# Kernel optimization log

Measured on AMD Instinct MI355X. Metric: run time of the kernel, lower is better.

The kernel has to match this reference:

```python
import jax, jax.numpy as jnp
import numpy as np

B, S, H = 16, 4096, 4096
NH, NKV, HD = 32, 8, 128
NREP = NH // NKV
EPS = 1e-5


def _rmsnorm(x, eps=EPS):
    xf = x.astype(jnp.float32)
    return (xf * jax.lax.rsqrt(jnp.mean(xf * xf, axis=-1, keepdims=True) + eps)).astype(x.dtype)


def setup_inputs() -> dict:
    key = jax.random.key(0)
    ks = jax.random.split(key, 8)
    x = jax.random.normal(ks[0], (B, 1, H), dtype=jnp.float32)
    last_pos = jax.random.randint(ks[1], (B,), 0, S)
    # rope cache: [max_seq, head_dim//2, 2] = stacked (cos, sin)
    inv_freq = 1.0 / (10000.0 ** (jnp.arange(0, HD, 2, dtype=jnp.float32) / HD))  # [HD//2]
    t = jnp.arange(S, dtype=jnp.float32)
    ang = t[:, None] * inv_freq[None, :]  # [S, HD//2]
    rope_cache = jnp.stack([jnp.cos(ang), jnp.sin(ang)], axis=-1)  # [S, HD//2, 2]
    mask = jnp.ones((B, 1, 1, S), dtype=bool)
    sc = 1.0 / np.sqrt(H)
    wqkv = jax.random.normal(ks[2], ((NH + 2 * NKV) * HD, H), dtype=jnp.float32) * sc
    o_proj_w = jax.random.normal(ks[3], (H, NH * HD), dtype=jnp.float32) * sc
    cache_k = jax.random.normal(ks[4], (B, S, NKV, HD), dtype=jnp.float32)
    cache_v = jax.random.normal(ks[5], (B, S, NKV, HD), dtype=jnp.float32)
    return {"x": x, "last_pos": last_pos, "rope_cache": rope_cache, "mask": mask,
            "wqkv": wqkv, "o_proj_w": o_proj_w, "cache_k": cache_k, "cache_v": cache_v}


def _rope_decode(x, last_pos, rope_cache):
    # x: [B, 1, nh, HD]; rope_cache: [S, HD//2, 2]; last_pos: [B]
    rc = rope_cache[last_pos]  # [B, HD//2, 2] gathered per position
    rc = rc[:, None, None, :, :]  # [B,1,1,HD//2,2]
    xs = x.astype(jnp.float32).reshape(*x.shape[:-1], HD // 2, 2)
    real = xs[..., 0] * rc[..., 0] - xs[..., 1] * rc[..., 1]
    imag = xs[..., 1] * rc[..., 0] + xs[..., 0] * rc[..., 1]
    return jnp.stack([real, imag], axis=-1).reshape(x.shape).astype(x.dtype)


def reference(x, last_pos, rope_cache, mask, wqkv, o_proj_w, cache_k, cache_v):
    bsz = x.shape[0]
    qkv = jnp.einsum('bsh,oh->bso', x, wqkv)  # [B,1,(NH+2*NKV)*HD]
    q_end = NH * HD
    k_end = q_end + NKV * HD
    q = qkv[..., :q_end].reshape(bsz, 1, NH, HD)
    k = qkv[..., q_end:k_end].reshape(bsz, 1, NKV, HD)
    v = qkv[..., k_end:].reshape(bsz, 1, NKV, HD)
    # RoPE at position last_pos (decode path: start_pos = last_pos)
    q = _rope_decode(q, last_pos, rope_cache)
    k = _rope_decode(k, last_pos, rope_cache)
    # QK RMSNorm over head_dim
    q = _rmsnorm(q)
    k = _rmsnorm(k)
    # scatter new K/V into cache at last_pos
    b_idx = jnp.arange(bsz)
    keys = cache_k.at[b_idx, last_pos].set(k[:, 0])    # [B,S,NKV,HD]
    values = cache_v.at[b_idx, last_pos].set(v[:, 0])  # [B,S,NKV,HD]
    # GQA attention without materializing repeat_interleave:
    # head h uses kv group h // NREP, so reshape heads -> [NKV, NREP]
    qg = q[:, 0].reshape(bsz, NKV, NREP, HD)
    scores = jnp.einsum('bgrd,bsgd->bgrs', qg, keys) / np.sqrt(HD)  # [B,NKV,NREP,S]
    neg = jnp.finfo(scores.dtype).min
    scores = jnp.where(mask, scores, neg)  # mask [B,1,1,S] broadcasts
    probs = jax.nn.softmax(scores.astype(jnp.float32), axis=-1).astype(q.dtype)
    out = jnp.einsum('bgrs,bsgd->bgrd', probs, values)  # [B,NKV,NREP,HD]
    out = out.reshape(bsz, 1, NH * HD)
    return jnp.einsum('bso,ho->bsh', out, o_proj_w)  # [B,1,H]
```

## Files before the change

kernel.cpp:

```cpp
#include <hip/hip_runtime.h>
#include <hip/hip_bf16.h>

#define BATCH   16
#define SEQ     4096
#define HID     4096
#define NHEADS  32
#define NKVH    8
#define HDIM    128
#define NREPS   4
#define QKV_DIM 6144
#define NSCH    16
#define SCH     256

__device__ __forceinline__ void gload16(float* lds, const float* g) {
  __builtin_amdgcn_global_load_lds(
      (const __attribute__((address_space(1))) unsigned int*)g,
      (__attribute__((address_space(3))) unsigned int*)lds,
      16, 0, 0);
}
#define WAITV(N) asm volatile("s_waitcnt vmcnt(" #N ")" ::: "memory")

__global__ __launch_bounds__(256) void gemv16(
    const float4* __restrict__ x4,
    const float4* __restrict__ w4,
    float* __restrict__ ypart,
    int M)
{
  const int wid  = threadIdx.x >> 6;
  const int lane = threadIdx.x & 63;
  const int mb   = M / 16;
  const int ks   = blockIdx.x / mb;
  const int rb   = blockIdx.x % mb;
  const int row0 = rb * 16 + wid * 4;
  const int k0   = ks * 512;

  float acc[16][4];
#pragma unroll
  for (int b = 0; b < 16; ++b) { acc[b][0]=0.f; acc[b][1]=0.f; acc[b][2]=0.f; acc[b][3]=0.f; }

  for (int c = 0; c < 512; c += 64) {
    const int kk = k0 + c + lane;
    const long wb = (long)row0 * 1024 + kk;
    float4 w0 = w4[wb];
    float4 w1 = w4[wb + 1024];
    float4 w2 = w4[wb + 2048];
    float4 w3 = w4[wb + 3072];
    float4 xv[16];
#pragma unroll
    for (int b = 0; b < 16; ++b) xv[b] = x4[(b << 10) + kk];
#pragma unroll
    for (int b = 0; b < 16; ++b) {
      acc[b][0] = fmaf(w0.x,xv[b].x,fmaf(w0.y,xv[b].y,fmaf(w0.z,xv[b].z,fmaf(w0.w,xv[b].w,acc[b][0]))));
      acc[b][1] = fmaf(w1.x,xv[b].x,fmaf(w1.y,xv[b].y,fmaf(w1.z,xv[b].z,fmaf(w1.w,xv[b].w,acc[b][1]))));
      acc[b][2] = fmaf(w2.x,xv[b].x,fmaf(w2.y,xv[b].y,fmaf(w2.z,xv[b].z,fmaf(w2.w,xv[b].w,acc[b][2]))));
      acc[b][3] = fmaf(w3.x,xv[b].x,fmaf(w3.y,xv[b].y,fmaf(w3.z,xv[b].z,fmaf(w3.w,xv[b].w,acc[b][3]))));
    }
  }
#pragma unroll
  for (int b = 0; b < 16; ++b) {
#pragma unroll
    for (int r = 0; r < 4; ++r) {
      float v = acc[b][r];
#pragma unroll
      for (int o = 32; o; o >>= 1) v += __shfl_xor(v, o, 64);
      if (lane == 0) ypart[((long)(ks * 16 + b)) * M + row0 + r] = v;
    }
  }
}

__global__ __launch_bounds__(64) void rope_rms(
    const float*  __restrict__ qp0,
    const float*  __restrict__ qp1,
    const int*    __restrict__ last_pos,
    const float2* __restrict__ rope2,
    float* __restrict__ proc)
{
  const int b    = blockIdx.x / 48;
  const int hh   = blockIdx.x % 48;
  const int lane = threadIdx.x;
  const int off  = b * QKV_DIM + hh * HDIM;

  float2 e0 = ((const float2*)(qp0 + off))[lane];
  float2 e1 = ((const float2*)(qp1 + off))[lane];
  float ex = e0.x + e1.x, ey = e0.y + e1.y;
  float r0 = ex, r1 = ey;
  if (hh < 40) {
    const int pos = last_pos[b];
    float2 cs = rope2[pos * 64 + lane];
    r0 = ex * cs.x - ey * cs.y;
    r1 = ey * cs.x + ex * cs.y;
    float ss = r0 * r0 + r1 * r1;
#pragma unroll
    for (int o = 32; o; o >>= 1) ss += __shfl_xor(ss, o, 64);
    float scl = rsqrtf(ss * (1.0f / 128.0f) + 1e-5f);
    r0 *= scl; r1 *= scl;
  }
  ((float2*)(proc + off))[lane] = make_float2(r0, r1);
}

__global__ __launch_bounds__(256, 4) void attn_partial(
    const float* __restrict__ proc,
    const float* __restrict__ cache_k,
    const float* __restrict__ cache_v,
    const int*   __restrict__ last_pos,
    float* __restrict__ part_out,
    float* __restrict__ part_ml)
{
  __shared__ float smem[8192];
  __shared__ float sc[NREPS][SCH];
  __shared__ float red[NREPS][8];

  const int ch  = blockIdx.x & (NSCH - 1);
  const int g   = (blockIdx.x >> 4) & 7;
  const int b   = blockIdx.x >> 7;
  const int tid = threadIdx.x;
  const int w   = tid >> 6;
  const int hw  = tid >> 5;
  const int h   = hw & 1;
  const int sub = tid & 31;
  const int r   = sub >> 3;
  const int sl  = sub & 7;
  const int pos = last_pos[b];
  const int s0  = ch * SCH;

  const float* kbase = cache_k + ((long)(b * SEQ) * NKVH + g) * HDIM;
  const float* vbase = cache_v + ((long)(b * SEQ) * NKVH + g) * HDIM;
  const float* knew  = proc + b * QKV_DIM + (NHEADS + g) * HDIM;
  const float* vnew  = proc + b * QKV_DIM + (NHEADS + NKVH + g) * HDIM;

  const float isq = 0.08838834764831845f;
  float4 ql[4];
#pragma unroll
  for (int t = 0; t < 4; ++t) {
    float4 q = *(const float4*)(proc + b * QKV_DIM + (g * NREPS + r) * HDIM + sl * 16 + t * 4);
    ql[t] = make_float4(q.x * isq, q.y * isq, q.z * isq, q.w * isq);
  }
  WAITV(0);

#define STAGE_K(tt, bf) do {                                                 \
    float* dst_ = &smem[((w * 2 + (bf)) * 8) * 128];                         \
    _Pragma("unroll")                                                        \
    for (int c_ = 0; c_ < 4; ++c_) {                                         \
      const int s_ = s0 + (w << 6) + ((tt) << 3) + (c_ << 1) + h;            \
      const float* src_ = (s_ == pos) ? (knew + (sub << 2))                  \
                                      : (kbase + (long)s_ * 1024 + (sub << 2)); \
      gload16(dst_ + (c_ << 8), src_);                                       \
    }                                                                        \
  } while (0)

#define STAGE_V(tt, bf) do {                                                 \
    float* dst_ = &smem[((w * 2 + (bf)) * 4) * 128];                         \
    { const int s_ = s0 + (w << 6) + ((tt) << 1) + h;                        \
      const float* src_ = (s_ == pos) ? (vnew + (sub << 2))                  \
                                      : (vbase + (long)s_ * 1024 + (sub << 2)); \
      gload16(dst_, src_); }                                                 \
    { const int s_ = s0 + (w << 6) + 32 + ((tt) << 1) + h;                   \
      const float* src_ = (s_ == pos) ? (vnew + (sub << 2))                  \
                                      : (vbase + (long)s_ * 1024 + (sub << 2)); \
      gload16(dst_ + 256, src_); }                                           \
  } while (0)

  STAGE_K(0, 0);
  STAGE_K(1, 1);
  float m = -3e38f;
  for (int tt = 0; tt < 8; ++tt) {
    if (tt < 7) WAITV(4); else WAITV(0);
    const float* kb = &smem[((w * 2 + (tt & 1)) * 8) * 128];
#pragma unroll
    for (int pp = 0; pp < 4; ++pp) {
      const int p = (pp << 1) + h;
      const float4 k0 = *(const float4*)&kb[p * 128 + sl * 16];
      const float4 k1 = *(const float4*)&kb[p * 128 + sl * 16 + 4];
      const float4 k2 = *(const float4*)&kb[p * 128 + sl * 16 + 8];
      const float4 k3 = *(const float4*)&kb[p * 128 + sl * 16 + 12];
      float d = k0.x*ql[0].x + k0.y*ql[0].y + k0.z*ql[0].z + k0.w*ql[0].w
              + k1.x*ql[1].x + k1.y*ql[1].y + k1.z*ql[1].z + k1.w*ql[1].w
              + k2.x*ql[2].x + k2.y*ql[2].y + k2.z*ql[2].z + k2.w*ql[2].w
              + k3.x*ql[3].x + k3.y*ql[3].y + k3.z*ql[3].z + k3.w*ql[3].w;
      d += __shfl_xor(d, 1); d += __shfl_xor(d, 2); d += __shfl_xor(d, 4);
      const int i = (w << 6) + (tt << 3) + p;
      if (sl == 0) sc[r][i] = d;
      m = fmaxf(m, d);
    }
    if (tt < 6) STAGE_K(tt + 2, tt & 1);
  }
  if (sl == 0) red[r][hw] = m;
  __syncthreads();

  STAGE_V(0, 0);
  STAGE_V(1, 1);

  float m_r[4];
#pragma unroll
  for (int r2 = 0; r2 < 4; ++r2) {
    float mm = red[r2][0];
#pragma unroll
    for (int h2 = 1; h2 < 8; ++h2) mm = fmaxf(mm, red[r2][h2]);
    m_r[r2] = mm;
  }

  float lsum[4];
  {
    const int i = tid;
#pragma unroll
    for (int r2 = 0; r2 < 4; ++r2) {
      float e = __expf(sc[r2][i] - m_r[r2]);
      sc[r2][i] = e;
      lsum[r2] = e;
    }
  }
  __syncthreads();
  const int wid  = tid >> 6;
  const int lane = tid & 63;
#pragma unroll
  for (int r2 = 0; r2 < 4; ++r2) {
    float v = lsum[r2];
#pragma unroll
    for (int o = 32; o; o >>= 1) v += __shfl_xor(v, o, 64);
    if (lane == 0) red[r2][wid] = v;
  }
  __syncthreads();
  float l_r[4];
#pragma unroll
  for (int r2 = 0; r2 < 4; ++r2)
    l_r[r2] = (red[r2][0] + red[r2][1]) + (red[r2][2] + red[r2][3]);

  float* ps = &smem[4096];
  const int dq = sub;
  float4 a0 = {0,0,0,0}, a1 = {0,0,0,0}, a2 = {0,0,0,0}, a3 = {0,0,0,0};
  for (int tt = 0; tt < 16; ++tt) {
    if (tt < 15) WAITV(2); else WAITV(0);
    const float* vb = &smem[((w * 2 + (tt & 1)) * 4) * 128];
#pragma unroll
    for (int j = 0; j < 2; ++j) {
      const int i = (w << 6) + (h << 5) + (tt << 1) + j;
      const float4 vv = *(const float4*)&vb[(h * 2 + j) * 128 + (dq << 2)];
      const float p0 = sc[0][i], p1 = sc[1][i], p2 = sc[2][i], p3 = sc[3][i];
      a0.x += p0*vv.x; a0.y += p0*vv.y; a0.z += p0*vv.z; a0.w += p0*vv.w;
      a1.x += p1*vv.x; a1.y += p1*vv.y; a1.z += p1*vv.z; a1.w += p1*vv.w;
      a2.x += p2*vv.x; a2.y += p2*vv.y; a2.z += p2*vv.z; a2.w += p2*vv.w;
      a3.x += p3*vv.x; a3.y += p3*vv.y; a3.z += p3*vv.z; a3.w += p3*vv.w;
    }
    if (tt < 14) STAGE_V(tt + 2, tt & 1);
  }
  *(float4*)&ps[(long)hw * 512 + 0 * 128 + (dq << 2)] = a0;
  *(float4*)&ps[(long)hw * 512 + 1 * 128 + (dq << 2)] = a1;
  *(float4*)&ps[(long)hw * 512 + 2 * 128 + (dq << 2)] = a2;
  *(float4*)&ps[(long)hw * 512 + 3 * 128 + (dq << 2)] = a3;
  __syncthreads();

  const long base = ((((long)b * NKVH + g) * NSCH + ch) * NREPS) * HDIM;
  for (int idx = tid; idx < 512; idx += 256) {
    float v = 0.f;
#pragma unroll
    for (int s2 = 0; s2 < 8; ++s2) v += ps[(long)s2 * 512 + idx];
    part_out[base + idx] = v;
  }
  if (tid < 4) {
    float mm = tid==0 ? m_r[0] : tid==1 ? m_r[1] : tid==2 ? m_r[2] : m_r[3];
    float ll = tid==0 ? l_r[0] : tid==1 ? l_r[1] : tid==2 ? l_r[2] : l_r[3];
    const long mlb = (((((long)b * NKVH + g) * NSCH + ch) * NREPS) + tid) * 2;
    part_ml[mlb]     = mm;
    part_ml[mlb + 1] = ll;
  }
#undef STAGE_K
#undef STAGE_V
}

__global__ __launch_bounds__(128) void attn_combine(
    const float* __restrict__ part_out,
    const float* __restrict__ part_ml,
    float* __restrict__ attn_out)
{
  const int r = blockIdx.x & 3;
  const int g = (blockIdx.x >> 2) & 7;
  const int b = blockIdx.x >> 5;
  const int d = threadIdx.x;

  float M = -3e38f;
#pragma unroll
  for (int c = 0; c < NSCH; ++c) {
    const long idx = ((((long)b * NKVH + g) * NSCH + c) * NREPS + r) * 2;
    M = fmaxf(M, part_ml[idx]);
  }
  float L = 0.f, o = 0.f;
#pragma unroll
  for (int c = 0; c < NSCH; ++c) {
    const long idx = ((((long)b * NKVH + g) * NSCH + c) * NREPS + r) * 2;
    const float w = __expf(part_ml[idx] - M);
    L += part_ml[idx + 1] * w;
    o += w * part_out[((((long)b * NKVH + g) * NSCH + c) * NREPS + r) * HDIM + d];
  }
  attn_out[((long)b * NHEADS + g * NREPS + r) * HDIM + d] = o / L;
}

__global__ __launch_bounds__(256) void gemv_oproj(
    const float4* __restrict__ x4,
    const float4* __restrict__ w4,
    float* __restrict__ out)
{
  const int wid  = threadIdx.x >> 6;
  const int lane = threadIdx.x & 63;
  const int row0 = blockIdx.x * 8 + wid * 2;

  float acc[16][2];
#pragma unroll
  for (int b = 0; b < 16; ++b) { acc[b][0] = 0.f; acc[b][1] = 0.f; }

  for (int c = 0; c < 1024; c += 64) {
    const int kk = c + lane;
    const long wb = (long)row0 * 1024 + kk;
    float4 w0 = w4[wb];
    float4 w1 = w4[wb + 1024];
    float4 xv[16];
#pragma unroll
    for (int b = 0; b < 16; ++b) xv[b] = x4[(b << 10) + kk];
#pragma unroll
    for (int b = 0; b < 16; ++b) {
      acc[b][0] = fmaf(w0.x,xv[b].x,fmaf(w0.y,xv[b].y,fmaf(w0.z,xv[b].z,fmaf(w0.w,xv[b].w,acc[b][0]))));
      acc[b][1] = fmaf(w1.x,xv[b].x,fmaf(w1.y,xv[b].y,fmaf(w1.z,xv[b].z,fmaf(w1.w,xv[b].w,acc[b][1]))));
    }
  }
#pragma unroll
  for (int b = 0; b < 16; ++b) {
#pragma unroll
    for (int r = 0; r < 2; ++r) {
      float v = acc[b][r];
#pragma unroll
      for (int o = 32; o; o >>= 1) v += __shfl_xor(v, o, 64);
      if (lane == 0) out[((long)b << 12) + row0 + r] = v;
    }
  }
}

extern "C" void kernel_launch(void* const* d_in, const int* in_sizes, int n_in,
                              void* d_out, int out_size, void* d_ws, size_t ws_size,
                              hipStream_t stream) {
  const float* x          = (const float*)d_in[0];
  const int*   last_pos   = (const int*)  d_in[1];
  const float* rope_cache = (const float*)d_in[2];
  const float* wqkv       = (const float*)d_in[4];
  const float* o_proj_w   = (const float*)d_in[5];
  const float* cache_k    = (const float*)d_in[6];
  const float* cache_v    = (const float*)d_in[7];
  float* out = (float*)d_out;
  float* ws  = (float*)d_ws;

  float* qkv_part = ws;
  float* proc     = ws + 196608;
  float* part_out = ws + 294912;
  float* part_ml  = ws + 1343488;
  float* attn_out = ws + 1359872;

  gemv16<<<(QKV_DIM / 16) * 2, 256, 0, stream>>>(
      (const float4*)x, (const float4*)wqkv, qkv_part, QKV_DIM);
  rope_rms<<<BATCH * 48, 64, 0, stream>>>(
      qkv_part, qkv_part + BATCH * QKV_DIM, last_pos,
      (const float2*)rope_cache, proc);
  attn_partial<<<BATCH * NKVH * NSCH, 256, 0, stream>>>(
      proc, cache_k, cache_v, last_pos, part_out, part_ml);
  attn_combine<<<BATCH * NKVH * NREPS, 128, 0, stream>>>(
      part_out, part_ml, attn_out);
  gemv_oproj<<<HID / 8, 256, 0, stream>>>(
      (const float4*)attn_out, (const float4*)o_proj_w, out);
}
```

Measured before the change: 208.6 us.

## Make each wave an independent attention split to remove block-level syncs

Each wave in the attention partial kernel now processes its own 64-position chunk with private staging buffers and score storage. Max and sum reductions use wave shuffles instead of shared-memory barriers, and V prefetch starts during the last K iterations. Partial results per wave are written out, so the combine kernel merges 64 chunks instead of 16. This removes __syncthreads and the cross-wave LDS reduction, at the cost of four times more partial output traffic and more combine work.

```diff
diff --git a/kernel.cpp b/kernel.cpp
--- a/kernel.cpp
+++ b/kernel.cpp
@@ -10,7 +10,7 @@
 #define NREPS   4
 #define QKV_DIM 6144
 #define NSCH    16
-#define SCH     256
+#define NCHW    64
 
 __device__ __forceinline__ void gload16(float* lds, const float* g) {
   __builtin_amdgcn_global_load_lds(
@@ -106,22 +106,24 @@
     float* __restrict__ part_out,
     float* __restrict__ part_ml)
 {
-  __shared__ float smem[8192];
-  __shared__ float sc[NREPS][SCH];
-  __shared__ float red[NREPS][8];
+  __shared__ float stage[4][2][1024];
+  __shared__ float scb[4][NREPS][64];
 
   const int ch  = blockIdx.x & (NSCH - 1);
   const int g   = (blockIdx.x >> 4) & 7;
   const int b   = blockIdx.x >> 7;
   const int tid = threadIdx.x;
   const int w   = tid >> 6;
-  const int hw  = tid >> 5;
-  const int h   = hw & 1;
+  const int h   = (tid >> 5) & 1;
   const int sub = tid & 31;
   const int r   = sub >> 3;
   const int sl  = sub & 7;
   const int pos = last_pos[b];
-  const int s0  = ch * SCH;
+  const int s0  = (ch << 8) + (w << 6);
+  const int chw = (ch << 2) + w;
+
+  float* kv = &stage[w][0][0];
+  float (*sc)[64] = scb[w];
 
   const float* kbase = cache_k + ((long)(b * SEQ) * NKVH + g) * HDIM;
   const float* vbase = cache_v + ((long)(b * SEQ) * NKVH + g) * HDIM;
@@ -132,139 +134,111 @@
   float4 ql[4];
 #pragma unroll
   for (int t = 0; t < 4; ++t) {
-    float4 q = *(const float4*)(proc + b * QKV_DIM + (g * NREPS + r) * HDIM + sl * 16 + t * 4);
+    float4 q = *(const float4*)(proc + b * QKV_DIM + (g * NREPS + r) * HDIM + t * 32 + sl * 4);
     ql[t] = make_float4(q.x * isq, q.y * isq, q.z * isq, q.w * isq);
   }
   WAITV(0);
 
-#define STAGE_K(tt, bf) do {                                                 \
-    float* dst_ = &smem[((w * 2 + (bf)) * 8) * 128];                         \
+#define STAGE(base_, new_, tt, bf) do {                                      \
+    float* dst_ = kv + (bf) * 1024;                                          \
     _Pragma("unroll")                                                        \
     for (int c_ = 0; c_ < 4; ++c_) {                                         \
-      const int s_ = s0 + (w << 6) + ((tt) << 3) + (c_ << 1) + h;            \
-      const float* src_ = (s_ == pos) ? (knew + (sub << 2))                  \
-                                      : (kbase + (long)s_ * 1024 + (sub << 2)); \
+      const int s_ = s0 + ((tt) << 3) + (h << 2) + c_;                       \
+      const float* src_ = (s_ == pos) ? ((new_) + (sub << 2))                \
+                                      : ((base_) + (long)s_ * 1024 + (sub << 2)); \
       gload16(dst_ + (c_ << 8), src_);                                       \
     }                                                                        \
   } while (0)
 
-#define STAGE_V(tt, bf) do {                                                 \
-    float* dst_ = &smem[((w * 2 + (bf)) * 4) * 128];                         \
-    { const int s_ = s0 + (w << 6) + ((tt) << 1) + h;                        \
-      const float* src_ = (s_ == pos) ? (vnew + (sub << 2))                  \
-                                      : (vbase + (long)s_ * 1024 + (sub << 2)); \
-      gload16(dst_, src_); }                                                 \
-    { const int s_ = s0 + (w << 6) + 32 + ((tt) << 1) + h;                   \
-      const float* src_ = (s_ == pos) ? (vnew + (sub << 2))                  \
-                                      : (vbase + (long)s_ * 1024 + (sub << 2)); \
-      gload16(dst_ + 256, src_); }                                           \
-  } while (0)
-
-  STAGE_K(0, 0);
-  STAGE_K(1, 1);
+  STAGE(kbase, knew, 0, 0);
+  STAGE(kbase, knew, 1, 1);
   float m = -3e38f;
+#pragma unroll
   for (int tt = 0; tt < 8; ++tt) {
-    if (tt < 7) WAITV(4); else WAITV(0);
-    const float* kb = &smem[((w * 2 + (tt & 1)) * 8) * 128];
+    WAITV(4);
+    const float* kb = kv + (tt & 1) * 1024;
 #pragma unroll
     for (int pp = 0; pp < 4; ++pp) {
-      const int p = (pp << 1) + h;
-      const float4 k0 = *(const float4*)&kb[p * 128 + sl * 16];
-      const float4 k1 = *(const float4*)&kb[p * 128 + sl * 16 + 4];
-      const float4 k2 = *(const float4*)&kb[p * 128 + sl * 16 + 8];
-      const float4 k3 = *(const float4*)&kb[p * 128 + sl * 16 + 12];
+      const float* row = kb + pp * 256 + h * 128 + sl * 4;
+      float4 k0 = *(const float4*)(row);
+      float4 k1 = *(const float4*)(row + 32);
+      float4 k2 = *(const float4*)(row + 64);
+      float4 k3 = *(const float4*)(row + 96);
       float d = k0.x*ql[0].x + k0.y*ql[0].y + k0.z*ql[0].z + k0.w*ql[0].w
               + k1.x*ql[1].x + k1.y*ql[1].y + k1.z*ql[1].z + k1.w*ql[1].w
               + k2.x*ql[2].x + k2.y*ql[2].y + k2.z*ql[2].z + k2.w*ql[2].w
               + k3.x*ql[3].x + k3.y*ql[3].y + k3.z*ql[3].z + k3.w*ql[3].w;
       d += __shfl_xor(d, 1); d += __shfl_xor(d, 2); d += __shfl_xor(d, 4);
-      const int i = (w << 6) + (tt << 3) + p;
-      if (sl == 0) sc[r][i] = d;
+      if (sl == 0) sc[r][(tt << 3) + (h << 2) + pp] = d;
       m = fmaxf(m, d);
     }
-    if (tt < 6) STAGE_K(tt + 2, tt & 1);
-  }
-  if (sl == 0) red[r][hw] = m;
-  __syncthreads();
-
-  STAGE_V(0, 0);
-  STAGE_V(1, 1);
-
-  float m_r[4];
-#pragma unroll
-  for (int r2 = 0; r2 < 4; ++r2) {
-    float mm = red[r2][0];
-#pragma unroll
-    for (int h2 = 1; h2 < 8; ++h2) mm = fmaxf(mm, red[r2][h2]);
-    m_r[r2] = mm;
-  }
-
-  float lsum[4];
+    if (tt < 6)      STAGE(kbase, knew, tt + 2, tt & 1);
+    else             STAGE(vbase, vnew, tt - 6, tt & 1);
+  }
+
+  m = fmaxf(m, __shfl_xor(m, 32));
+  m = fmaxf(m, __shfl_xor(m, 1));
+  m = fmaxf(m, __shfl_xor(m, 2));
+  m = fmaxf(m, __shfl_xor(m, 4));
+
+  float lsum;
   {
-    const int i = tid;
-#pragma unroll
-    for (int r2 = 0; r2 < 4; ++r2) {
-      float e = __expf(sc[r2][i] - m_r[r2]);
-      sc[r2][i] = e;
-      lsum[r2] = e;
-    }
-  }
-  __syncthreads();
-  const int wid  = tid >> 6;
-  const int lane = tid & 63;
-#pragma unroll
-  for (int r2 = 0; r2 < 4; ++r2) {
-    float v = lsum[r2];
-#pragma unroll
-    for (int o = 32; o; o >>= 1) v += __shfl_xor(v, o, 64);
-    if (lane == 0) red[r2][wid] = v;
-  }
-  __syncthreads();
-  float l_r[4];
-#pragma unroll
-  for (int r2 = 0; r2 < 4; ++r2)
-    l_r[r2] = (red[r2][0] + red[r2][1]) + (red[r2][2] + red[r2][3]);
-
-  float* ps = &smem[4096];
+    const int i0 = (sl << 3) + (h << 2);
+    float4 e4 = *(const float4*)&sc[r][i0];
+    e4.x = __expf(e4.x - m); e4.y = __expf(e4.y - m);
+    e4.z = __expf(e4.z - m); e4.w = __expf(e4.w - m);
+    *(float4*)&sc[r][i0] = e4;
+    lsum = (e4.x + e4.y) + (e4.z + e4.w);
+  }
+  lsum += __shfl_xor(lsum, 32);
+  lsum += __shfl_xor(lsum, 1);
+  lsum += __shfl_xor(lsum, 2);
+  lsum += __shfl_xor(lsum, 4);
+
+  if (h == 0 && sl == 0) {
+    const long mlb = ((((long)(b * NKVH + g)) * NCHW + chw) * NREPS + r) * 2;
+    part_ml[mlb]     = m;
+    part_ml[mlb + 1] = lsum;
+  }
+
   const int dq = sub;
   float4 a0 = {0,0,0,0}, a1 = {0,0,0,0}, a2 = {0,0,0,0}, a3 = {0,0,0,0};
-  for (int tt = 0; tt < 16; ++tt) {
-    if (tt < 15) WAITV(2); else WAITV(0);
-    const float* vb = &smem[((w * 2 + (tt & 1)) * 4) * 128];
-#pragma unroll
-    for (int j = 0; j < 2; ++j) {
-      const int i = (w << 6) + (h << 5) + (tt << 1) + j;
-      const float4 vv = *(const float4*)&vb[(h * 2 + j) * 128 + (dq << 2)];
-      const float p0 = sc[0][i], p1 = sc[1][i], p2 = sc[2][i], p3 = sc[3][i];
-      a0.x += p0*vv.x; a0.y += p0*vv.y; a0.z += p0*vv.z; a0.w += p0*vv.w;
-      a1.x += p1*vv.x; a1.y += p1*vv.y; a1.z += p1*vv.z; a1.w += p1*vv.w;
-      a2.x += p2*vv.x; a2.y += p2*vv.y; a2.z += p2*vv.z; a2.w += p2*vv.w;
-      a3.x += p3*vv.x; a3.y += p3*vv.y; a3.z += p3*vv.z; a3.w += p3*vv.w;
-    }
-    if (tt < 14) STAGE_V(tt + 2, tt & 1);
-  }
-  *(float4*)&ps[(long)hw * 512 + 0 * 128 + (dq << 2)] = a0;
-  *(float4*)&ps[(long)hw * 512 + 1 * 128 + (dq << 2)] = a1;
-  *(float4*)&ps[(long)hw * 512 + 2 * 128 + (dq << 2)] = a2;
-  *(float4*)&ps[(long)hw * 512 + 3 * 128 + (dq << 2)] = a3;
-  __syncthreads();
-
-  const long base = ((((long)b * NKVH + g) * NSCH + ch) * NREPS) * HDIM;
-  for (int idx = tid; idx < 512; idx += 256) {
-    float v = 0.f;
-#pragma unroll
-    for (int s2 = 0; s2 < 8; ++s2) v += ps[(long)s2 * 512 + idx];
-    part_out[base + idx] = v;
-  }
-  if (tid < 4) {
-    float mm = tid==0 ? m_r[0] : tid==1 ? m_r[1] : tid==2 ? m_r[2] : m_r[3];
-    float ll = tid==0 ? l_r[0] : tid==1 ? l_r[1] : tid==2 ? l_r[2] : l_r[3];
-    const long mlb = (((((long)b * NKVH + g) * NSCH + ch) * NREPS) + tid) * 2;
-    part_ml[mlb]     = mm;
-    part_ml[mlb + 1] = ll;
-  }
-#undef STAGE_K
-#undef STAGE_V
+#pragma unroll
+  for (int tt = 0; tt < 8; ++tt) {
+    if (tt < 7) WAITV(4); else WAITV(0);
+    const float* vb = kv + (tt & 1) * 1024;
+    const int i0 = (tt << 3) + (h << 2);
+    const float4 p0 = *(const float4*)&sc[0][i0];
+    const float4 p1 = *(const float4*)&sc[1][i0];
+    const float4 p2 = *(const float4*)&sc[2][i0];
+    const float4 p3 = *(const float4*)&sc[3][i0];
+#pragma unroll
+    for (int c = 0; c < 4; ++c) {
+      const float4 vv = *(const float4*)(vb + c * 256 + h * 128 + (dq << 2));
+      const float q0 = ((const float*)&p0)[c];
+      const float q1 = ((const float*)&p1)[c];
+      const float q2 = ((const float*)&p2)[c];
+      const float q3 = ((const float*)&p3)[c];
+      a0.x += q0*vv.x; a0.y += q0*vv.y; a0.z += q0*vv.z; a0.w += q0*vv.w;
+      a1.x += q1*vv.x; a1.y += q1*vv.y; a1.z += q1*vv.z; a1.w += q1*vv.w;
+      a2.x += q2*vv.x; a2.y += q2*vv.y; a2.z += q2*vv.z; a2.w += q2*vv.w;
+      a3.x += q3*vv.x; a3.y += q3*vv.y; a3.z += q3*vv.z; a3.w += q3*vv.w;
+    }
+    if (tt < 6) STAGE(vbase, vnew, tt + 2, tt & 1);
+  }
+
+#pragma unroll
+  for (int k = 0; k < 4; ++k) {
+    float4* ak = k==0 ? &a0 : k==1 ? &a1 : k==2 ? &a2 : &a3;
+    ak->x += __shfl_xor(ak->x, 32);
+    ak->y += __shfl_xor(ak->y, 32);
+    ak->z += __shfl_xor(ak->z, 32);
+    ak->w += __shfl_xor(ak->w, 32);
+  }
+  float* pb = part_out + ((((long)(b * NKVH + g)) * NCHW + chw) * NREPS) * HDIM + (dq << 2);
+  *(float4*)(pb + (h * 2 + 0) * HDIM) = h ? a2 : a0;
+  *(float4*)(pb + (h * 2 + 1) * HDIM) = h ? a3 : a1;
+#undef STAGE
 }
 
 __global__ __launch_bounds__(128) void attn_combine(
@@ -276,20 +250,20 @@
   const int g = (blockIdx.x >> 2) & 7;
   const int b = blockIdx.x >> 5;
   const int d = threadIdx.x;
+  const long gb = (long)(b * NKVH + g);
 
   float M = -3e38f;
-#pragma unroll
-  for (int c = 0; c < NSCH; ++c) {
-    const long idx = ((((long)b * NKVH + g) * NSCH + c) * NREPS + r) * 2;
-    M = fmaxf(M, part_ml[idx]);
-  }
+#pragma unroll 8
+  for (int c = 0; c < NCHW; ++c)
+    M = fmaxf(M, part_ml[((gb * NCHW + c) * NREPS + r) * 2]);
+
   float L = 0.f, o = 0.f;
-#pragma unroll
-  for (int c = 0; c < NSCH; ++c) {
-    const long idx = ((((long)b * NKVH + g) * NSCH + c) * NREPS + r) * 2;
-    const float w = __expf(part_ml[idx] - M);
-    L += part_ml[idx + 1] * w;
-    o += w * part_out[((((long)b * NKVH + g) * NSCH + c) * NREPS + r) * HDIM + d];
+#pragma unroll 8
+  for (int c = 0; c < NCHW; ++c) {
+    const long idx = ((gb * NCHW + c) * NREPS + r) * 2;
+    const float wgt = __expf(part_ml[idx] - M);
+    L += part_ml[idx + 1] * wgt;
+    o += wgt * part_out[((gb * NCHW + c) * NREPS + r) * HDIM + d];
   }
   attn_out[((long)b * NHEADS + g * NREPS + r) * HDIM + d] = o / L;
 }
@@ -349,8 +323,8 @@
   float* qkv_part = ws;
   float* proc     = ws + 196608;
   float* part_out = ws + 294912;
-  float* part_ml  = ws + 1343488;
-  float* attn_out = ws + 1359872;
+  float* part_ml  = ws + 4489216;
+  float* attn_out = ws + 4554752;
 
   gemv16<<<(QKV_DIM / 16) * 2, 256, 0, stream>>>(
       (const float4*)x, (const float4*)wqkv, qkv_part, QKV_DIM);
```

Measured after the change: 259.4 us. 1.24x slower.

## Stage GEMV activations in LDS and split K four ways for both projections

Applied to the files above, without the earlier changes.

The QKV GEMV now stages the 16-batch activation slice in shared memory, so each wave reads it from LDS instead of issuing 16 global float4 loads per step. K is split into four chunks of 1024 instead of two, which doubles the grid, and rope_rms sums four partials. The o_proj GEMV reuses the same split-K kernel, followed by a new add4 reduction kernel. This buys more parallelism and less redundant activation traffic, at the cost of an extra launch and extra partial-sum traffic.

```diff
diff --git a/kernel.cpp b/kernel.cpp
--- a/kernel.cpp
+++ b/kernel.cpp
@@ -20,40 +20,46 @@
 }
 #define WAITV(N) asm volatile("s_waitcnt vmcnt(" #N ")" ::: "memory")
 
-__global__ __launch_bounds__(256) void gemv16(
+__global__ __launch_bounds__(256) void gemv_ldsx(
     const float4* __restrict__ x4,
     const float4* __restrict__ w4,
     float* __restrict__ ypart,
     int M)
 {
+  constexpr int KC4 = 256;
+  __shared__ float4 xs[16][KC4];
   const int wid  = threadIdx.x >> 6;
   const int lane = threadIdx.x & 63;
   const int mb   = M / 16;
   const int ks   = blockIdx.x / mb;
   const int rb   = blockIdx.x % mb;
   const int row0 = rb * 16 + wid * 4;
-  const int k0   = ks * 512;
+  const int k0   = ks * KC4;
+
+#pragma unroll
+  for (int i = threadIdx.x; i < 16 * KC4; i += 256)
+    xs[i >> 8][i & 255] = x4[((i >> 8) << 10) + k0 + (i & 255)];
+  __syncthreads();
 
   float acc[16][4];
 #pragma unroll
   for (int b = 0; b < 16; ++b) { acc[b][0]=0.f; acc[b][1]=0.f; acc[b][2]=0.f; acc[b][3]=0.f; }
 
-  for (int c = 0; c < 512; c += 64) {
+#pragma unroll
+  for (int c = 0; c < KC4; c += 64) {
     const int kk = k0 + c + lane;
     const long wb = (long)row0 * 1024 + kk;
     float4 w0 = w4[wb];
     float4 w1 = w4[wb + 1024];
     float4 w2 = w4[wb + 2048];
     float4 w3 = w4[wb + 3072];
-    float4 xv[16];
-#pragma unroll
-    for (int b = 0; b < 16; ++b) xv[b] = x4[(b << 10) + kk];
 #pragma unroll
     for (int b = 0; b < 16; ++b) {
-      acc[b][0] = fmaf(w0.x,xv[b].x,fmaf(w0.y,xv[b].y,fmaf(w0.z,xv[b].z,fmaf(w0.w,xv[b].w,acc[b][0]))));
-      acc[b][1] = fmaf(w1.x,xv[b].x,fmaf(w1.y,xv[b].y,fmaf(w1.z,xv[b].z,fmaf(w1.w,xv[b].w,acc[b][1]))));
-      acc[b][2] = fmaf(w2.x,xv[b].x,fmaf(w2.y,xv[b].y,fmaf(w2.z,xv[b].z,fmaf(w2.w,xv[b].w,acc[b][2]))));
-      acc[b][3] = fmaf(w3.x,xv[b].x,fmaf(w3.y,xv[b].y,fmaf(w3.z,xv[b].z,fmaf(w3.w,xv[b].w,acc[b][3]))));
+      float4 xv = xs[b][c + lane];
+      acc[b][0] = fmaf(w0.x,xv.x,fmaf(w0.y,xv.y,fmaf(w0.z,xv.z,fmaf(w0.w,xv.w,acc[b][0]))));
+      acc[b][1] = fmaf(w1.x,xv.x,fmaf(w1.y,xv.y,fmaf(w1.z,xv.z,fmaf(w1.w,xv.w,acc[b][1]))));
+      acc[b][2] = fmaf(w2.x,xv.x,fmaf(w2.y,xv.y,fmaf(w2.z,xv.z,fmaf(w2.w,xv.w,acc[b][2]))));
+      acc[b][3] = fmaf(w3.x,xv.x,fmaf(w3.y,xv.y,fmaf(w3.z,xv.z,fmaf(w3.w,xv.w,acc[b][3]))));
     }
   }
 #pragma unroll
@@ -68,9 +74,8 @@
   }
 }
 
-__global__ __launch_bounds__(64) void rope_rms(
-    const float*  __restrict__ qp0,
-    const float*  __restrict__ qp1,
+__global__ __launch_bounds__(64) void rope_rms4(
+    const float*  __restrict__ qp,
     const int*    __restrict__ last_pos,
     const float2* __restrict__ rope2,
     float* __restrict__ proc)
@@ -80,9 +85,12 @@
   const int lane = threadIdx.x;
   const int off  = b * QKV_DIM + hh * HDIM;
 
-  float2 e0 = ((const float2*)(qp0 + off))[lane];
-  float2 e1 = ((const float2*)(qp1 + off))[lane];
-  float ex = e0.x + e1.x, ey = e0.y + e1.y;
+  float ex = 0.f, ey = 0.f;
+#pragma unroll
+  for (int s = 0; s < 4; ++s) {
+    float2 t = ((const float2*)(qp + (long)s * BATCH * QKV_DIM + off))[lane];
+    ex += t.x; ey += t.y;
+  }
   float r0 = ex, r1 = ey;
   if (hh < 40) {
     const int pos = last_pos[b];
@@ -294,42 +302,14 @@
   attn_out[((long)b * NHEADS + g * NREPS + r) * HDIM + d] = o / L;
 }
 
-__global__ __launch_bounds__(256) void gemv_oproj(
-    const float4* __restrict__ x4,
-    const float4* __restrict__ w4,
-    float* __restrict__ out)
-{
-  const int wid  = threadIdx.x >> 6;
-  const int lane = threadIdx.x & 63;
-  const int row0 = blockIdx.x * 8 + wid * 2;
-
-  float acc[16][2];
-#pragma unroll
-  for (int b = 0; b < 16; ++b) { acc[b][0] = 0.f; acc[b][1] = 0.f; }
-
-  for (int c = 0; c < 1024; c += 64) {
-    const int kk = c + lane;
-    const long wb = (long)row0 * 1024 + kk;
-    float4 w0 = w4[wb];
-    float4 w1 = w4[wb + 1024];
-    float4 xv[16];
-#pragma unroll
-    for (int b = 0; b < 16; ++b) xv[b] = x4[(b << 10) + kk];
-#pragma unroll
-    for (int b = 0; b < 16; ++b) {
-      acc[b][0] = fmaf(w0.x,xv[b].x,fmaf(w0.y,xv[b].y,fmaf(w0.z,xv[b].z,fmaf(w0.w,xv[b].w,acc[b][0]))));
-      acc[b][1] = fmaf(w1.x,xv[b].x,fmaf(w1.y,xv[b].y,fmaf(w1.z,xv[b].z,fmaf(w1.w,xv[b].w,acc[b][1]))));
-    }
-  }
-#pragma unroll
-  for (int b = 0; b < 16; ++b) {
-#pragma unroll
-    for (int r = 0; r < 2; ++r) {
-      float v = acc[b][r];
-#pragma unroll
-      for (int o = 32; o; o >>= 1) v += __shfl_xor(v, o, 64);
-      if (lane == 0) out[((long)b << 12) + row0 + r] = v;
-    }
+__global__ __launch_bounds__(256) void add4(
+    const float4* __restrict__ p, float4* __restrict__ o, int n4)
+{
+  int i = blockIdx.x * 256 + threadIdx.x;
+  if (i < n4) {
+    float4 a = p[i], b = p[i + n4], c = p[i + 2 * n4], d = p[i + 3 * n4];
+    o[i] = make_float4(a.x+b.x+c.x+d.x, a.y+b.y+c.y+d.y,
+                       a.z+b.z+c.z+d.z, a.w+b.w+c.w+d.w);
   }
 }
 
@@ -347,20 +327,22 @@
   float* ws  = (float*)d_ws;
 
   float* qkv_part = ws;
-  float* proc     = ws + 196608;
-  float* part_out = ws + 294912;
-  float* part_ml  = ws + 1343488;
-  float* attn_out = ws + 1359872;
-
-  gemv16<<<(QKV_DIM / 16) * 2, 256, 0, stream>>>(
+  float* proc     = ws + 393216;
+  float* part_out = ws + 491520;
+  float* part_ml  = ws + 1540096;
+  float* attn_out = ws + 1556480;
+  float* out_part = ws + 1622016;
+
+  gemv_ldsx<<<(QKV_DIM / 16) * 4, 256, 0, stream>>>(
       (const float4*)x, (const float4*)wqkv, qkv_part, QKV_DIM);
-  rope_rms<<<BATCH * 48, 64, 0, stream>>>(
-      qkv_part, qkv_part + BATCH * QKV_DIM, last_pos,
-      (const float2*)rope_cache, proc);
+  rope_rms4<<<BATCH * 48, 64, 0, stream>>>(
+      qkv_part, last_pos, (const float2*)rope_cache, proc);
   attn_partial<<<BATCH * NKVH * NSCH, 256, 0, stream>>>(
       proc, cache_k, cache_v, last_pos, part_out, part_ml);
   attn_combine<<<BATCH * NKVH * NREPS, 128, 0, stream>>>(
       part_out, part_ml, attn_out);
-  gemv_oproj<<<HID / 8, 256, 0, stream>>>(
-      (const float4*)attn_out, (const float4*)o_proj_w, out);
-}
+  gemv_ldsx<<<(HID / 16) * 4, 256, 0, stream>>>(
+      (const float4*)attn_out, (const float4*)o_proj_w, out_part, HID);
+  add4<<<(BATCH * HID / 4 + 255) / 256, 256, 0, stream>>>(
+      (const float4*)out_part, (float4*)out, BATCH * HID / 4);
+}
```

Measured after the change: 333.0 us. 1.6x slower.
